# Performance work log

Hardware: AMD Instinct MI355X
Metric: run time of the kernel (lower is better)

The kernel has to match this reference:

```python
import jax, jax.numpy as jnp
import numpy as np

B, RES, C = 32, 56, 128
HEADS, WS, NW = 4, 7, 8
HD = C // HEADS            # 32
NQ = NW * NW               # 64 windows
WA = WS * WS               # 49 tokens per window
TOPK = 64


def _topk_closest(q_win, k_win, topk):
    qh, qw = q_win; kh, kw = k_win
    ch_q = np.arange(qh); cw_q = np.arange(qw)
    if qh != kh:
        f = kh // qh
        ch_q = ch_q * f + f // 2
        cw_q = cw_q * f + f // 2
    cq = np.stack(np.meshgrid(ch_q, cw_q, indexing='ij'))              # (2,qh,qw)
    ck = np.stack(np.meshgrid(np.arange(kh), np.arange(kw), indexing='ij'))
    fq = cq.reshape(2, -1); fk = ck.reshape(2, -1)
    rel = fq[:, :, None] - fk[:, None, :]                               # (2,nQ,nK)
    dist = np.sqrt(rel[0].astype(np.float32) ** 2 + rel[1].astype(np.float32) ** 2)
    topk = min(topk, dist.shape[1])
    idx = np.argsort(dist, axis=1, kind='stable')[:, :topk]             # (nQ,topk)
    coord = np.take_along_axis(rel, np.broadcast_to(idx[None], (2,) + idx.shape), axis=2)
    return idx.astype(np.int32), coord.transpose(1, 2, 0).astype(np.float32)


def _buffers():
    # window-relative coords, same as register_buffer('window_coords')
    ch = np.arange(WS) - WS // 2
    wc = np.stack(np.meshgrid(ch, ch, indexing='ij'), axis=-1).reshape(-1, 2).astype(np.float32)  # (49,2)
    # level 0: fine grid (RES x RES); level 1: window grid (NW x NW)
    idx0, c0 = _topk_closest((NW, NW), (RES, RES), TOPK)
    idx1, c1 = _topk_closest((NW, NW), (NW, NW), TOPK)
    c1 = c1 * WS  # k > 0 coords scaled by window size
    coords0 = c0[:, None, :, :] + wc[None, :, None, :]   # (NQ,49,TOPK,2)
    coords1 = c1[:, None, :, :] + wc[None, :, None, :]
    return idx0, idx1, coords0, coords1


def setup_inputs() -> dict:
    key = jax.random.key(0)
    ks = jax.random.split(key, 16)
    idx0, idx1, coords0, coords1 = _buffers()
    s = 0.02
    return {
        'x0': jax.random.normal(ks[0], (B, RES, RES, C), jnp.float32),
        'x1': jax.random.normal(ks[1], (B, NQ, C), jnp.float32),
        'qkv_w': jax.random.normal(ks[2], (3 * C, C), jnp.float32) * s,
        'qkv_b': jnp.zeros((3 * C,), jnp.float32),
        'proj_w': jax.random.normal(ks[3], (C, C), jnp.float32) * s,
        'proj_b': jnp.zeros((C,), jnp.float32),
        'rpb0_w1': jax.random.normal(ks[4], (HD, 2), jnp.float32) * s,
        'rpb0_b1': jnp.zeros((HD,), jnp.float32),
        'rpb0_w2': jax.random.normal(ks[5], (HEADS, HD), jnp.float32) * s,
        'rpb0_b2': jnp.zeros((HEADS,), jnp.float32),
        'rpb1_w1': jax.random.normal(ks[6], (HD, 2), jnp.float32) * s,
        'rpb1_b1': jnp.zeros((HD,), jnp.float32),
        'rpb1_w2': jax.random.normal(ks[7], (HEADS, HD), jnp.float32) * s,
        'rpb1_b2': jnp.zeros((HEADS,), jnp.float32),
        'coords0': jnp.asarray(coords0),
        'coords1': jnp.asarray(coords1),
        'idx0': jnp.asarray(idx0),
        'idx1': jnp.asarray(idx1),
    }


def _rpb_mlp(coords, w1, b1, w2, b2):
    # (NQ,49,T,2) -> (NQ,49,T,heads)
    return jax.nn.relu(coords @ w1.T + b1) @ w2.T + b2


def _gather_kv(kv, idx_flat):
    # kv: (B,L,heads,hd); gathered -> (B,NQ,heads,TOPK,hd)
    g = kv[:, idx_flat]
    return g.reshape(kv.shape[0], NQ, TOPK, HEADS, HD).transpose(0, 1, 3, 2, 4)


def reference(x0, x1, qkv_w, qkv_b, proj_w, proj_b,
              rpb0_w1, rpb0_b1, rpb0_w2, rpb0_b2,
              rpb1_w1, rpb1_b1, rpb1_w2, rpb1_b2,
              coords0, coords1, idx0, idx1):
    b = x0.shape[0]
    scale = HD ** -0.5
    qkv = x0 @ qkv_w.T + qkv_b                       # (B,RES,RES,3C)
    q, k, v = jnp.split(qkv, 3, axis=-1)
    # window-partition q: (B,RES,RES,C) -> (B,NQ,heads,49,hd)
    qw = q.reshape(b, NW, WS, NW, WS, C).transpose(0, 1, 3, 2, 4, 5)
    qw = qw.reshape(b, NQ, WA, HEADS, HD).transpose(0, 1, 3, 2, 4)
    # level 0 KV from fine grid
    k0 = k.reshape(b, RES * RES, HEADS, HD)
    v0 = v.reshape(b, RES * RES, HEADS, HD)
    i0 = idx0.reshape(-1)
    k0s, v0s = _gather_kv(k0, i0), _gather_kv(v0, i0)
    # level 1 KV from pooled tokens (same qkv projection)
    qkv1 = (x1 @ qkv_w.T + qkv_b).reshape(b, NQ, 3, HEADS, HD)
    i1 = idx1.reshape(-1)
    k1s, v1s = _gather_kv(qkv1[:, :, 1], i1), _gather_kv(qkv1[:, :, 2], i1)
    k_all = jnp.concatenate([k0s, k1s], axis=3)      # (B,NQ,heads,2T,hd)
    v_all = jnp.concatenate([v0s, v1s], axis=3)
    attn = jnp.einsum('bqhnd,bqhmd->bqhnm', qw * scale, k_all)  # (B,NQ,heads,49,2T)
    rpb0 = _rpb_mlp(coords0, rpb0_w1, rpb0_b1, rpb0_w2, rpb0_b2)
    rpb1 = _rpb_mlp(coords1, rpb1_w1, rpb1_b1, rpb1_w2, rpb1_b2)
    rpb = jnp.concatenate([rpb0, rpb1], axis=2).transpose(0, 3, 1, 2)  # (NQ,heads,49,2T)
    attn = jax.nn.softmax(attn + rpb[None], axis=-1)
    out = jnp.einsum('bqhnm,bqhmd->bqhnd', attn, v_all)
    out = out.transpose(0, 1, 3, 2, 4).reshape(b * NQ, WA, C)
    return out @ proj_w.T + proj_b
```

## Files before the change

kernel.cpp:

```cpp
#include <hip/hip_runtime.h>
#include <hip/hip_bf16.h>


typedef __bf16 bf16_t;
typedef __bf16 bf16x8 __attribute__((ext_vector_type(8)));
typedef float f32x4 __attribute__((ext_vector_type(4)));

static __device__ __forceinline__ f32x4 mfma_bf16(bf16x8 a, bf16x8 b, f32x4 c) {
  return __builtin_amdgcn_mfma_f32_16x16x32_bf16(a, b, c, 0, 0, 0);
}

static __device__ __forceinline__ bf16x8 cvt8(const float* __restrict__ p) {
  float4 a = *(const float4*)p;
  float4 b = *(const float4*)(p + 4);
  bf16x8 r;
  r[0] = (bf16_t)a.x; r[1] = (bf16_t)a.y; r[2] = (bf16_t)a.z; r[3] = (bf16_t)a.w;
  r[4] = (bf16_t)b.x; r[5] = (bf16_t)b.y; r[6] = (bf16_t)b.z; r[7] = (bf16_t)b.w;
  return r;
}

#define NB 32
#define RES 56
#define CH 128
#define NW 8
#define NQ 64
#define WA 49
#define X0_ROWS (NB * RES * RES)
#define SCALE 0.17677669529663687f
#define SQRT32 5.656854249492381f
#define KE 0.25503164508761f

__global__ __launch_bounds__(256) void k_qkv(
    const float* __restrict__ x0, const float* __restrict__ x1,
    const float* __restrict__ w, const float* __restrict__ bias,
    bf16_t* __restrict__ qout,
    bf16_t* __restrict__ k0, bf16_t* __restrict__ v0,
    bf16_t* __restrict__ k1, bf16_t* __restrict__ v1) {
  __shared__ __align__(16) bf16_t Asm[64][136];
  __shared__ __align__(16) bf16_t Bsm[128][136];
  const int rb = blockIdx.x;
  const int tid = threadIdx.x;
  const size_t row0 = (size_t)rb * 64;
  const bool is_x0 = (rb < 1568);
  const int b_ = rb / 49;
  const int pix0 = (rb - b_ * 49) * 64;
  const int i1base = (rb - 1568) * 64;

  const float* src = is_x0 ? (x0 + row0 * CH)
                           : (x1 + (row0 - X0_ROWS) * CH);
#pragma unroll
  for (int i = 0; i < 4; ++i) {
    int uid = tid + 256 * i;
    int r = uid >> 4, cs = uid & 15;
    *(bf16x8*)&Asm[r][cs * 8] = cvt8(src + (size_t)r * CH + cs * 8);
  }

  const int wid = tid >> 6, l = tid & 63;
  const int lr = l & 15, lkg = l >> 4, lk = lkg * 8;

  for (int cb = 0; cb < 3; ++cb) {
    const float* wsrc = w + (size_t)cb * 128 * CH;
#pragma unroll
    for (int i = 0; i < 8; ++i) {
      int uid = tid + 256 * i;
      int r = uid >> 4, cs = uid & 15;
      *(bf16x8*)&Bsm[r][cs * 8] = cvt8(wsrc + (size_t)r * CH + cs * 8);
    }
    __syncthreads();

    f32x4 zero = {0.f, 0.f, 0.f, 0.f};
    f32x4 acc[8];
#pragma unroll
    for (int nt = 0; nt < 8; ++nt) acc[nt] = zero;
#pragma unroll
    for (int ks = 0; ks < 4; ++ks) {
      bf16x8 a = *(const bf16x8*)&Asm[wid * 16 + lr][ks * 32 + lk];
#pragma unroll
      for (int nt = 0; nt < 8; ++nt) {
        bf16x8 b = *(const bf16x8*)&Bsm[nt * 16 + lr][ks * 32 + lk];
        acc[nt] = mfma_bf16(a, b, acc[nt]);
      }
    }
    float bias_v[8];
#pragma unroll
    for (int nt = 0; nt < 8; ++nt) bias_v[nt] = bias[cb * 128 + nt * 16 + lr];

#pragma unroll
    for (int r4 = 0; r4 < 4; ++r4) {
      int local = wid * 16 + lkg * 4 + r4;
      if (is_x0) {
        int pix = pix0 + local;
        int rr = pix / 56, cc = pix - rr * 56;
        if (cb == 0) {
          int wn = b_ * 64 + (rr / 7) * 8 + cc / 7;
          int nidx = (rr % 7) * 7 + (cc % 7);
          bf16_t* dst = qout + (size_t)wn * 12544 + nidx * 128;
#pragma unroll
          for (int nt = 0; nt < 8; ++nt)
            dst[nt * 16 + lr] = (bf16_t)(acc[nt][r4] + bias_v[nt]);
        } else {
          bf16_t* dst = (cb == 1 ? k0 : v0) +
                        ((size_t)b_ * 3136 + pix) * CH;
#pragma unroll
          for (int nt = 0; nt < 8; ++nt)
            dst[nt * 16 + lr] = (bf16_t)(acc[nt][r4] + bias_v[nt]);
        }
      } else if (cb != 0) {
        bf16_t* dst = (cb == 1 ? k1 : v1) + (size_t)(i1base + local) * CH;
#pragma unroll
        for (int nt = 0; nt < 8; ++nt)
          dst[nt * 16 + lr] = (bf16_t)(acc[nt][r4] + bias_v[nt]);
      }
    }
    __syncthreads();
  }
}

__global__ __launch_bounds__(256) void k_rpb(
    const float* __restrict__ c0, const float* __restrict__ c1,
    const float* __restrict__ w10, const float* __restrict__ b10,
    const float* __restrict__ w20, const float* __restrict__ b20,
    const float* __restrict__ w11, const float* __restrict__ b11,
    const float* __restrict__ w21, const float* __restrict__ b21,
    float* __restrict__ rpb) {
  __shared__ float w1s[2][32][2], b1s[2][32], w2s[2][4][32], b2s[2][4];
  const int tid = threadIdx.x;
  if (tid < 64) {
    int s = tid >> 5, j = tid & 31;
    const float* w1p = s ? w11 : w10;
    const float* b1p = s ? b11 : b10;
    w1s[s][j][0] = w1p[j * 2];
    w1s[s][j][1] = w1p[j * 2 + 1];
    b1s[s][j] = b1p[j];
  }
  {
    int s = tid >> 7, rem = tid & 127, h = rem >> 5, j = rem & 31;
    w2s[s][h][j] = s ? w21[h * 32 + j] : w20[h * 32 + j];
  }
  if (tid < 8) {
    int s = tid >> 2, h = tid & 3;
    b2s[s][h] = s ? b21[h] : b20[h];
  }
  __syncthreads();

  int L = blockIdx.x * 256 + tid;
  int m = L & 127;
  int n = (L >> 7) % WA;
  int qi = L / (128 * WA);
  int s = m >> 6, mi = m & 63;
  const float* cp = (s ? c1 : c0) + (((size_t)qi * WA + n) * 64 + mi) * 2;
  float cx = cp[0], cy = cp[1];
  float a0 = 0.f, a1 = 0.f, a2 = 0.f, a3 = 0.f;
#pragma unroll
  for (int j = 0; j < 32; ++j) {
    float h = fmaxf(w1s[s][j][0] * cx + w1s[s][j][1] * cy + b1s[s][j], 0.f);
    a0 += w2s[s][0][j] * h;
    a1 += w2s[s][1][j] * h;
    a2 += w2s[s][2][j] * h;
    a3 += w2s[s][3][j] * h;
  }
  size_t base = ((size_t)qi * 4 * WA + n) * 128 + m;
  rpb[base] = (a0 + b2s[s][0]) * SQRT32;
  rpb[base + (size_t)WA * 128] = (a1 + b2s[s][1]) * SQRT32;
  rpb[base + (size_t)2 * WA * 128] = (a2 + b2s[s][2]) * SQRT32;
  rpb[base + (size_t)3 * WA * 128] = (a3 + b2s[s][3]) * SQRT32;
}

__global__ __launch_bounds__(256, 4) void k_attn(
    const bf16_t* qin,
    const bf16_t* __restrict__ k0, const bf16_t* __restrict__ v0,
    const bf16_t* __restrict__ k1, const bf16_t* __restrict__ v1,
    const int* __restrict__ idx0, const int* __restrict__ idx1,
    const float* __restrict__ rpb,
    float* attn_out) {
  __shared__ __align__(16) bf16_t Kt[128][72];
  __shared__ __align__(16) bf16_t Vt[64][136];
  bf16_t (*Sm)[136] = (bf16_t(*)[136])&Kt[0][0];

  const int bid = blockIdx.x;
  const int hp = bid & 1;
  const int qi = (bid >> 1) & 63;
  const int b = bid >> 7;
  const int tid = threadIdx.x;
  const int wn = b * 64 + qi;

#pragma unroll
  for (int i = 0; i < 4; ++i) {
    int uid = tid + 256 * i;
    int key = uid & 127, seg = uid >> 7;
    size_t srcrow;
    const bf16_t *kbase, *vbase;
    if (key < 64) {
      srcrow = (size_t)b * 3136 + idx0[qi * 64 + key];
      kbase = k0; vbase = v0;
    } else {
      srcrow = (size_t)b * 64 + idx1[qi * 64 + key - 64];
      kbase = k1; vbase = v1;
    }
    size_t off = srcrow * CH + hp * 64 + seg * 8;
    *(uint4*)&Kt[key][seg * 8] = *(const uint4*)(kbase + off);
    union { uint4 u; bf16_t h[8]; } cv;
    cv.u = *(const uint4*)(vbase + off);
#pragma unroll
    for (int e = 0; e < 8; ++e) Vt[seg * 8 + e][key] = cv.h[e];
  }

  const int wid = tid >> 6, l = tid & 63;
  const int lr = l & 15, lkg = l >> 4, lk = lkg * 8;
  const int myrow = wid * 16 + lkg * 4;
  int qr = wid * 16 + lr;
  if (qr > WA - 1) qr = WA - 1;

  const bf16_t* qb = qin + (size_t)wn * 12544;
  bf16x8 qf[2];
  qf[0] = *(const bf16x8*)&qb[qr * 128 + hp * 64 + lk];
  qf[1] = *(const bf16x8*)&qb[qr * 128 + hp * 64 + 32 + lk];

  f32x4 acc[2][8];
#pragma unroll
  for (int lh = 0; lh < 2; ++lh) {
    const float* rp = rpb + ((size_t)(qi * 4 + hp * 2 + lh) * WA) * 128;
#pragma unroll
    for (int nt = 0; nt < 8; ++nt)
#pragma unroll
      for (int r4 = 0; r4 < 4; ++r4)
        acc[lh][nt][r4] = rp[(myrow + r4) * 128 + nt * 16 + lr];
  }

  __syncthreads();

#pragma unroll
  for (int lh = 0; lh < 2; ++lh)
#pragma unroll
    for (int nt = 0; nt < 8; ++nt) {
      bf16x8 bfr = *(const bf16x8*)&Kt[nt * 16 + lr][lh * 32 + lk];
      acc[lh][nt] = mfma_bf16(qf[lh], bfr, acc[lh][nt]);
    }

  __syncthreads();

  float* obase = attn_out + (size_t)wn * 6272;

#pragma unroll
  for (int lh = 0; lh < 2; ++lh) {
    const int hh = hp * 2 + lh;
    float mx[4] = {-1e30f, -1e30f, -1e30f, -1e30f};
#pragma unroll
    for (int nt = 0; nt < 8; ++nt)
#pragma unroll
      for (int r4 = 0; r4 < 4; ++r4) mx[r4] = fmaxf(mx[r4], acc[lh][nt][r4]);
#pragma unroll
    for (int m = 1; m < 16; m <<= 1)
#pragma unroll
      for (int r4 = 0; r4 < 4; ++r4)
        mx[r4] = fmaxf(mx[r4], __shfl_xor(mx[r4], m));
    float km[4];
#pragma unroll
    for (int r4 = 0; r4 < 4; ++r4) km[r4] = KE * mx[r4];
    float sum[4] = {0.f, 0.f, 0.f, 0.f};
#pragma unroll
    for (int nt = 0; nt < 8; ++nt)
#pragma unroll
      for (int r4 = 0; r4 < 4; ++r4) {
        float p = __builtin_amdgcn_exp2f(fmaf(KE, acc[lh][nt][r4], -km[r4]));
        acc[lh][nt][r4] = p;
        sum[r4] += p;
      }
#pragma unroll
    for (int m = 1; m < 16; m <<= 1)
#pragma unroll
      for (int r4 = 0; r4 < 4; ++r4) sum[r4] += __shfl_xor(sum[r4], m);
    float inv[4];
#pragma unroll
    for (int r4 = 0; r4 < 4; ++r4) inv[r4] = __builtin_amdgcn_rcpf(sum[r4]);
#pragma unroll
    for (int nt = 0; nt < 8; ++nt)
#pragma unroll
      for (int r4 = 0; r4 < 4; ++r4)
        Sm[myrow + r4][nt * 16 + lr] = (bf16_t)acc[lh][nt][r4];
    f32x4 zero = {0.f, 0.f, 0.f, 0.f};
    f32x4 oacc[2];
    oacc[0] = zero; oacc[1] = zero;
#pragma unroll
    for (int ks = 0; ks < 4; ++ks) {
      bf16x8 pa = *(const bf16x8*)&Sm[wid * 16 + lr][ks * 32 + lk];
#pragma unroll
      for (int nt2 = 0; nt2 < 2; ++nt2) {
        bf16x8 vb = *(const bf16x8*)&Vt[lh * 32 + nt2 * 16 + lr][ks * 32 + lk];
        oacc[nt2] = mfma_bf16(pa, vb, oacc[nt2]);
      }
    }
#pragma unroll
    for (int nt2 = 0; nt2 < 2; ++nt2)
#pragma unroll
      for (int r4 = 0; r4 < 4; ++r4) {
        int rown = myrow + r4;
        if (rown < WA)
          obase[rown * 128 + hh * 32 + nt2 * 16 + lr] = oacc[nt2][r4] * inv[r4];
      }
  }
}

__global__ __launch_bounds__(256) void k_proj(
    const float* attn,
    const float* __restrict__ pw, const float* __restrict__ pb,
    float* out) {
  __shared__ __align__(16) bf16_t Asm[64][136];
  __shared__ __align__(16) bf16_t Bsm[128][136];
  const int rb = blockIdx.x;
  const int tid = threadIdx.x;
  const size_t row0 = (size_t)rb * 64;
#pragma unroll
  for (int i = 0; i < 4; ++i) {
    int uid = tid + 256 * i;
    int r = uid >> 4, cs = uid & 15;
    *(bf16x8*)&Asm[r][cs * 8] = cvt8(attn + (row0 + r) * CH + cs * 8);
  }
#pragma unroll
  for (int i = 0; i < 8; ++i) {
    int uid = tid + 256 * i;
    int r = uid >> 4, cs = uid & 15;
    *(bf16x8*)&Bsm[r][cs * 8] = cvt8(pw + (size_t)r * CH + cs * 8);
  }
  __syncthreads();

  const int wid = tid >> 6, l = tid & 63;
  const int lr = l & 15, lkg = l >> 4, lk = lkg * 8;
  f32x4 zero = {0.f, 0.f, 0.f, 0.f};
  f32x4 acc[8];
#pragma unroll
  for (int nt = 0; nt < 8; ++nt) acc[nt] = zero;
#pragma unroll
  for (int ks = 0; ks < 4; ++ks) {
    bf16x8 a = *(const bf16x8*)&Asm[wid * 16 + lr][ks * 32 + lk];
#pragma unroll
    for (int nt = 0; nt < 8; ++nt) {
      bf16x8 b = *(const bf16x8*)&Bsm[nt * 16 + lr][ks * 32 + lk];
      acc[nt] = mfma_bf16(a, b, acc[nt]);
    }
  }
#pragma unroll
  for (int nt = 0; nt < 8; ++nt) {
    int n = nt * 16 + lr;
    float bs = pb[n];
#pragma unroll
    for (int r4 = 0; r4 < 4; ++r4) {
      size_t g = row0 + (size_t)(wid * 16 + lkg * 4 + r4);
      out[g * CH + n] = acc[nt][r4] + bs;
    }
  }
}

extern "C" void kernel_launch(void* const* d_in, const int* in_sizes, int n_in,
                              void* d_out, int out_size, void* d_ws, size_t ws_size,
                              hipStream_t stream) {
  const float* x0 = (const float*)d_in[0];
  const float* x1 = (const float*)d_in[1];
  const float* qkv_w = (const float*)d_in[2];
  const float* qkv_b = (const float*)d_in[3];
  const float* proj_w = (const float*)d_in[4];
  const float* proj_b = (const float*)d_in[5];
  const float* rpb0_w1 = (const float*)d_in[6];
  const float* rpb0_b1 = (const float*)d_in[7];
  const float* rpb0_w2 = (const float*)d_in[8];
  const float* rpb0_b2 = (const float*)d_in[9];
  const float* rpb1_w1 = (const float*)d_in[10];
  const float* rpb1_b1 = (const float*)d_in[11];
  const float* rpb1_w2 = (const float*)d_in[12];
  const float* rpb1_b2 = (const float*)d_in[13];
  const float* coords0 = (const float*)d_in[14];
  const float* coords1 = (const float*)d_in[15];
  const int* idx0 = (const int*)d_in[16];
  const int* idx1 = (const int*)d_in[17];

  char* ws = (char*)d_ws;
  bf16_t* k0 = (bf16_t*)(ws + 0);
  bf16_t* v0 = (bf16_t*)(ws + 25690112);
  bf16_t* k1 = (bf16_t*)(ws + 51380224);
  bf16_t* v1 = (bf16_t*)(ws + 51904512);
  float* rpb = (float*)(ws + 52428800);

  k_qkv<<<1600, 256, 0, stream>>>(x0, x1, qkv_w, qkv_b,
                                  (bf16_t*)d_out, k0, v0, k1, v1);
  k_rpb<<<1568, 256, 0, stream>>>(coords0, coords1, rpb0_w1, rpb0_b1, rpb0_w2,
                                  rpb0_b2, rpb1_w1, rpb1_b1, rpb1_w2, rpb1_b2,
                                  rpb);
  k_attn<<<4096, 256, 0, stream>>>((const bf16_t*)d_out, k0, v0, k1, v1,
                                   idx0, idx1, rpb, (float*)d_out);
  k_proj<<<1568, 256, 0, stream>>>((const float*)d_out, proj_w, proj_b,
                                   (float*)d_out);
}
```

Before: 227.2 us.

## Pre-convert weights to bf16 and store relative position bias in fragment-ordered bf16

Adds a small prep kernel that converts the qkv and proj weights to bf16 once per call, so every GEMM block copies bf16 weights directly instead of converting fp32 each time. The relative position bias is now written as bf16 in a layout matching the MFMA accumulator fragment order. Each attention lane can then load its bias with four 16-byte vector loads instead of 64 scattered fp32 loads. This halves the bias footprint and cuts per-block weight traffic, at the cost of one extra launch and reduced bias precision.

```diff
diff --git a/kernel.cpp b/kernel.cpp
--- a/kernel.cpp
+++ b/kernel.cpp
@@ -30,9 +30,21 @@
 #define SQRT32 5.656854249492381f
 #define KE 0.25503164508761f
 
+__global__ __launch_bounds__(256) void k_prep(
+    const float* __restrict__ qw, const float* __restrict__ pw,
+    bf16_t* __restrict__ wq, bf16_t* __restrict__ wp) {
+  int i = (blockIdx.x * 256 + threadIdx.x) * 8;
+  if (i < 49152) {
+    *(bf16x8*)&wq[i] = cvt8(qw + i);
+  } else {
+    int j = i - 49152;
+    *(bf16x8*)&wp[j] = cvt8(pw + j);
+  }
+}
+
 __global__ __launch_bounds__(256) void k_qkv(
     const float* __restrict__ x0, const float* __restrict__ x1,
-    const float* __restrict__ w, const float* __restrict__ bias,
+    const bf16_t* __restrict__ w, const float* __restrict__ bias,
     bf16_t* __restrict__ qout,
     bf16_t* __restrict__ k0, bf16_t* __restrict__ v0,
     bf16_t* __restrict__ k1, bf16_t* __restrict__ v1) {
@@ -59,12 +71,12 @@
   const int lr = l & 15, lkg = l >> 4, lk = lkg * 8;
 
   for (int cb = 0; cb < 3; ++cb) {
-    const float* wsrc = w + (size_t)cb * 128 * CH;
+    const bf16_t* wsrc = w + (size_t)cb * 128 * CH;
 #pragma unroll
     for (int i = 0; i < 8; ++i) {
       int uid = tid + 256 * i;
       int r = uid >> 4, cs = uid & 15;
-      *(bf16x8*)&Bsm[r][cs * 8] = cvt8(wsrc + (size_t)r * CH + cs * 8);
+      *(uint4*)&Bsm[r][cs * 8] = *(const uint4*)(wsrc + (size_t)r * CH + cs * 8);
     }
     __syncthreads();
 
@@ -122,7 +134,7 @@
     const float* __restrict__ w20, const float* __restrict__ b20,
     const float* __restrict__ w11, const float* __restrict__ b11,
     const float* __restrict__ w21, const float* __restrict__ b21,
-    float* __restrict__ rpb) {
+    bf16_t* __restrict__ rpb) {
   __shared__ float w1s[2][32][2], b1s[2][32], w2s[2][4][32], b2s[2][4];
   const int tid = threadIdx.x;
   if (tid < 64) {
@@ -159,11 +171,12 @@
     a2 += w2s[s][2][j] * h;
     a3 += w2s[s][3][j] * h;
   }
-  size_t base = ((size_t)qi * 4 * WA + n) * 128 + m;
-  rpb[base] = (a0 + b2s[s][0]) * SQRT32;
-  rpb[base + (size_t)WA * 128] = (a1 + b2s[s][1]) * SQRT32;
-  rpb[base + (size_t)2 * WA * 128] = (a2 + b2s[s][2]) * SQRT32;
-  rpb[base + (size_t)3 * WA * 128] = (a3 + b2s[s][3]) * SQRT32;
+  size_t base = (size_t)(qi * 4) * 8192 +
+                (size_t)(((n >> 2) * 16 + (m & 15)) * 32 + (m >> 4) * 4 + (n & 3));
+  rpb[base]         = (bf16_t)((a0 + b2s[s][0]) * SQRT32);
+  rpb[base + 8192]  = (bf16_t)((a1 + b2s[s][1]) * SQRT32);
+  rpb[base + 16384] = (bf16_t)((a2 + b2s[s][2]) * SQRT32);
+  rpb[base + 24576] = (bf16_t)((a3 + b2s[s][3]) * SQRT32);
 }
 
 __global__ __launch_bounds__(256, 4) void k_attn(
@@ -171,7 +184,7 @@
     const bf16_t* __restrict__ k0, const bf16_t* __restrict__ v0,
     const bf16_t* __restrict__ k1, const bf16_t* __restrict__ v1,
     const int* __restrict__ idx0, const int* __restrict__ idx1,
-    const float* __restrict__ rpb,
+    const bf16_t* __restrict__ rpb,
     float* attn_out) {
   __shared__ __align__(16) bf16_t Kt[128][72];
   __shared__ __align__(16) bf16_t Vt[64][136];
@@ -219,12 +232,16 @@
   f32x4 acc[2][8];
 #pragma unroll
   for (int lh = 0; lh < 2; ++lh) {
-    const float* rp = rpb + ((size_t)(qi * 4 + hp * 2 + lh) * WA) * 128;
+    const bf16_t* rp = rpb + (size_t)(qi * 4 + hp * 2 + lh) * 8192 +
+                       (size_t)(((wid * 4 + lkg) * 16 + lr) * 32);
+    union { uint4 u[4]; bf16_t h[32]; } rv;
+#pragma unroll
+    for (int i = 0; i < 4; ++i) rv.u[i] = *(const uint4*)(rp + i * 8);
 #pragma unroll
     for (int nt = 0; nt < 8; ++nt)
 #pragma unroll
       for (int r4 = 0; r4 < 4; ++r4)
-        acc[lh][nt][r4] = rp[(myrow + r4) * 128 + nt * 16 + lr];
+        acc[lh][nt][r4] = (float)rv.h[nt * 4 + r4];
   }
 
   __syncthreads();
@@ -303,7 +320,7 @@
 
 __global__ __launch_bounds__(256) void k_proj(
     const float* attn,
-    const float* __restrict__ pw, const float* __restrict__ pb,
+    const bf16_t* __restrict__ pw, const float* __restrict__ pb,
     float* out) {
   __shared__ __align__(16) bf16_t Asm[64][136];
   __shared__ __align__(16) bf16_t Bsm[128][136];
@@ -320,7 +337,7 @@
   for (int i = 0; i < 8; ++i) {
     int uid = tid + 256 * i;
     int r = uid >> 4, cs = uid & 15;
-    *(bf16x8*)&Bsm[r][cs * 8] = cvt8(pw + (size_t)r * CH + cs * 8);
+    *(uint4*)&Bsm[r][cs * 8] = *(const uint4*)(pw + (size_t)r * CH + cs * 8);
   }
   __syncthreads();
 
@@ -378,15 +395,18 @@
   bf16_t* v0 = (bf16_t*)(ws + 25690112);
   bf16_t* k1 = (bf16_t*)(ws + 51380224);
   bf16_t* v1 = (bf16_t*)(ws + 51904512);
-  float* rpb = (float*)(ws + 52428800);
-
-  k_qkv<<<1600, 256, 0, stream>>>(x0, x1, qkv_w, qkv_b,
+  bf16_t* rpb = (bf16_t*)(ws + 52428800);
+  bf16_t* wq = (bf16_t*)(ws + 56623104);
+  bf16_t* wp = (bf16_t*)(ws + 56721408);
+
+  k_prep<<<32, 256, 0, stream>>>(qkv_w, proj_w, wq, wp);
+  k_qkv<<<1600, 256, 0, stream>>>(x0, x1, wq, qkv_b,
                                   (bf16_t*)d_out, k0, v0, k1, v1);
   k_rpb<<<1568, 256, 0, stream>>>(coords0, coords1, rpb0_w1, rpb0_b1, rpb0_w2,
                                   rpb0_b2, rpb1_w1, rpb1_b1, rpb1_w2, rpb1_b2,
                                   rpb);
   k_attn<<<4096, 256, 0, stream>>>((const bf16_t*)d_out, k0, v0, k1, v1,
                                    idx0, idx1, rpb, (float*)d_out);
-  k_proj<<<1568, 256, 0, stream>>>((const float*)d_out, proj_w, proj_b,
+  k_proj<<<1568, 256, 0, stream>>>((const float*)d_out, wp, proj_b,
                                    (float*)d_out);
 }
```

Measured after the change: 222.6 us. -2.0%, faster.
